# Performance work log

Measured on AMD Instinct MI355X. Metric: run time of the kernel, lower is better.

Reference implementation:

```python
import jax, jax.numpy as jnp
import numpy as np

N = 200000      # nodes (Elliptic-scale transaction graph)
E = 400000      # directed edges
F_IN = 165      # node features
HID = 128
OUT = 2


def setup_inputs() -> dict:
    key = jax.random.key(0)
    k = jax.random.split(key, 5)
    x = jax.random.normal(k[0], (N, F_IN), dtype=jnp.float32)
    edge_index = jax.random.randint(k[1], (2, E), 0, N, dtype=jnp.int32)
    # GCNConv params (PyG: Linear without bias semantics differ slightly by
    # version; here weight + bias, bias added after aggregation)
    W1 = jax.random.normal(k[2], (F_IN, HID), dtype=jnp.float32) * (1.0 / np.sqrt(F_IN))
    b1 = jnp.zeros((HID,), dtype=jnp.float32)
    W2 = jax.random.normal(k[3], (HID, OUT), dtype=jnp.float32) * (1.0 / np.sqrt(HID))
    b2 = jnp.zeros((OUT,), dtype=jnp.float32)
    return {"x": x, "edge_index": edge_index, "W1": W1, "b1": b1, "W2": W2, "b2": b2}


def _gcn_conv(h, edge_index, W, b):
    """PyG GCNConv: out = D^{-1/2} (A + I) D^{-1/2} (h @ W) + b."""
    h = h @ W                                    # [N, F_out]
    loop = jnp.arange(N, dtype=edge_index.dtype)
    src = jnp.concatenate([edge_index[0], loop])  # add self-loops
    dst = jnp.concatenate([edge_index[1], loop])
    # degree over destination nodes (self-loops guarantee deg >= 1)
    deg = jax.ops.segment_sum(jnp.ones_like(dst, dtype=h.dtype), dst, num_segments=N)
    dinv = jax.lax.rsqrt(deg)
    norm = dinv[src] * dinv[dst]                 # [E+N]
    msgs = h[src] * norm[:, None]                # gather + scale
    out = jax.ops.segment_sum(msgs, dst, num_segments=N)  # scatter-add
    return out + b


def reference(x, edge_index, W1, b1, W2, b2):
    h = _gcn_conv(x, edge_index, W1, b1)
    # torch.relu then F.dropout(training=False) (identity) then torch.relu:
    # in eval mode relu(relu(h)) == relu(h)
    h = jnp.maximum(h, 0.0)
    return _gcn_conv(h, edge_index, W2, b2)
```

## Files before the change

kernel.cpp:

```cpp
#include <hip/hip_runtime.h>
#include <hip/hip_bf16.h>

typedef __attribute__((ext_vector_type(8))) short bf16x8;
typedef __attribute__((ext_vector_type(4))) float f32x4;

#define N_NODES 200000
#define N_EDGES 400000
#define F_IN    165
#define HID     128
#define N_TILES 3125
#define KSTEPS  6
#define CAP     32

__device__ __forceinline__ uint bf16r(float f) {
  uint u = __float_as_uint(f);
  return (u + 0x7FFFu + ((u >> 16) & 1u)) >> 16;
}

__device__ __forceinline__ void gload16(const void* gp, void* lp) {
  __builtin_amdgcn_global_load_lds(
      (const __attribute__((address_space(1))) unsigned int*)gp,
      (__attribute__((address_space(3))) unsigned int*)lp, 16, 0, 0);
}


__global__ __launch_bounds__(256) void k_init(const float* __restrict__ W1,
                                              ushort* __restrict__ Wf,
                                              uint4* __restrict__ cursor) {
  int b = blockIdx.x;
  int tid = threadIdx.x;
  if (b < 96) {
    int id = b * 256 + tid;
    int j = id & 7;
    int lane = (id >> 3) & 63;
    int rem = id >> 9;
    int s = rem % 6;
    int ct = rem / 6;
    int k = s * 32 + (lane >> 4) * 8 + j;
    int col = ct * 16 + (lane & 15);
    float v = (k < F_IN) ? W1[k * HID + col] : 0.f;
    Wf[id] = (ushort)bf16r(v);
  } else {
    int i = (b - 96) * 256 + tid;
    if (i < 50000) cursor[i] = make_uint4(0, 0, 0, 0);
  }
}


__global__ __launch_bounds__(256) void k_gemm1p(const float* __restrict__ x,
                                                const ushort* __restrict__ Wf,
                                                const int* __restrict__ ei,
                                                int* __restrict__ cursor,
                                                int* __restrict__ slots,
                                                uint* __restrict__ g) {
  __shared__ float xs[64 * F_IN];
  const int tid  = threadIdx.x;
  const int wave = tid >> 6;
  const int lane = tid & 63;
  const int r15  = lane & 15;
  const int kg   = lane >> 4;

  if (tid < 128) {
    int e = blockIdx.x * 128 + tid;
    int d = ei[N_EDGES + e];
    int pos = atomicAdd(&cursor[d], 1);
    if (pos < CAP) slots[d * CAP + pos] = ei[e];
  }

  bf16x8 bfrag[2][KSTEPS];
  #pragma unroll
  for (int t = 0; t < 2; ++t) {
    int ct = wave * 2 + t;
    #pragma unroll
    for (int s = 0; s < KSTEPS; ++s)
      bfrag[t][s] = *(const bf16x8*)(Wf + (size_t)(((ct * KSTEPS + s) * 64 + lane) << 3));
  }

  const size_t tb = (size_t)blockIdx.x * (64 * F_IN);
  #pragma unroll
  for (int it = 0; it < 10; ++it) {
    gload16(x + tb + (size_t)(it * 256 + tid) * 4,
            (char*)xs + (size_t)(it * 256 + wave * 64) * 16);
  }
  if (tid < 80) {
    int c = 2560 + tid;
    *(float4*)((char*)xs + (size_t)c * 16) = *(const float4*)(x + tb + (size_t)c * 4);
  }
  __syncthreads();

  f32x4 acc[4][2];
  #pragma unroll
  for (int rg = 0; rg < 4; ++rg) {
    acc[rg][0] = (f32x4){0.f, 0.f, 0.f, 0.f};
    acc[rg][1] = (f32x4){0.f, 0.f, 0.f, 0.f};
  }

  #pragma unroll
  for (int rg = 0; rg < 4; ++rg) {
    const float* rp0 = xs + (rg * 16 + r15) * F_IN;
    #pragma unroll
    for (int s = 0; s < KSTEPS; ++s) {
      uint o0, o1, o2, o3;
      if (s < 5) {
        const float* rp = rp0 + s * 32 + kg * 8;
        o0 = bf16r(rp[0]) | (bf16r(rp[1]) << 16);
        o1 = bf16r(rp[2]) | (bf16r(rp[3]) << 16);
        o2 = bf16r(rp[4]) | (bf16r(rp[5]) << 16);
        o3 = bf16r(rp[6]) | (bf16r(rp[7]) << 16);
      } else {
        o0 = o1 = o2 = o3 = 0u;
        if (kg == 0) {
          const float* rp = rp0 + 160;
          o0 = bf16r(rp[0]) | (bf16r(rp[1]) << 16);
          o1 = bf16r(rp[2]) | (bf16r(rp[3]) << 16);
          o2 = bf16r(rp[4]);
        }
      }
      uint4 uu = make_uint4(o0, o1, o2, o3);
      bf16x8 a = *(bf16x8*)&uu;
      acc[rg][0] = __builtin_amdgcn_mfma_f32_16x16x32_bf16(a, bfrag[0][s], acc[rg][0], 0, 0, 0);
      acc[rg][1] = __builtin_amdgcn_mfma_f32_16x16x32_bf16(a, bfrag[1][s], acc[rg][1], 0, 0, 0);
    }
  }

  int base = blockIdx.x * 64;
  #pragma unroll
  for (int rg = 0; rg < 4; ++rg) {
    #pragma unroll
    for (int r = 0; r < 4; ++r) {
      int row = base + rg * 16 + kg * 4 + r;
      uint u = bf16r(acc[rg][0][r]) | (bf16r(acc[rg][1][r]) << 16);
      g[(size_t)row * 64 + wave * 16 + r15] = u;
    }
  }
}


__global__ __launch_bounds__(256) void k_agg1(const uint* __restrict__ g,
                                              const int* __restrict__ cursor,
                                              const int* __restrict__ slots,
                                              const float* __restrict__ b1,
                                              const float* __restrict__ W2,
                                              float* __restrict__ g2) {
  const int tid  = threadIdx.x;
  const int lane = tid & 63;
  const int wave = tid >> 6;
  const int sub  = lane >> 4;
  const int fl   = lane & 15;

  float  b1lo[4], b1hi[4];
  float2 w2lo[4], w2hi[4];
  #pragma unroll
  for (int k = 0; k < 4; ++k) {
    int dw = fl * 4 + k;
    int c0 = ((dw >> 4) << 5) + (dw & 15);
    b1lo[k] = b1[c0];
    b1hi[k] = b1[c0 + 16];
    w2lo[k] = *(const float2*)&W2[c0 * 2];
    w2hi[k] = *(const float2*)&W2[(c0 + 16) * 2];
  }

  int degs[8], slotv[8];
  #pragma unroll
  for (int it = 0; it < 8; ++it) {
    int node = blockIdx.x * 128 + it * 16 + wave * 4 + sub;
    int cn = min(node, N_NODES - 1);
    degs[it]  = cursor[cn];
    slotv[it] = slots[cn * CAP + fl];
  }

  #pragma unroll
  for (int it = 0; it < 8; ++it) {
    int node = blockIdx.x * 128 + it * 16 + wave * 4 + sub;
    if (node < N_NODES) {
      int deg = degs[it];
      float dv = rsqrtf(1.0f + (float)deg);
      int dcap = min(deg, 16);
      int srcl = (fl < dcap) ? slotv[it] : node;

      uint4 v = *(const uint4*)&g[(size_t)node * 64 + fl * 4];
      float sx0 = dv * __uint_as_float(v.x << 16), sy0 = dv * __uint_as_float(v.x & 0xFFFF0000u);
      float sx1 = dv * __uint_as_float(v.y << 16), sy1 = dv * __uint_as_float(v.y & 0xFFFF0000u);
      float sx2 = dv * __uint_as_float(v.z << 16), sy2 = dv * __uint_as_float(v.z & 0xFFFF0000u);
      float sx3 = dv * __uint_as_float(v.w << 16), sy3 = dv * __uint_as_float(v.w & 0xFFFF0000u);

      #pragma unroll
      for (int j = 0; j < 4; ++j) {
        int s = __shfl(srcl, sub * 16 + j);
        float wj = (j < dcap) ? rsqrtf(1.0f + (float)cursor[s]) : 0.f;
        uint4 w = *(const uint4*)&g[(size_t)s * 64 + fl * 4];
        sx0 = fmaf(__uint_as_float(w.x << 16), wj, sx0);
        sy0 = fmaf(__uint_as_float(w.x & 0xFFFF0000u), wj, sy0);
        sx1 = fmaf(__uint_as_float(w.y << 16), wj, sx1);
        sy1 = fmaf(__uint_as_float(w.y & 0xFFFF0000u), wj, sy1);
        sx2 = fmaf(__uint_as_float(w.z << 16), wj, sx2);
        sy2 = fmaf(__uint_as_float(w.z & 0xFFFF0000u), wj, sy2);
        sx3 = fmaf(__uint_as_float(w.w << 16), wj, sx3);
        sy3 = fmaf(__uint_as_float(w.w & 0xFFFF0000u), wj, sy3);
      }
      for (int j = 4; j < dcap; ++j) {
        int s = __shfl(srcl, sub * 16 + j);
        float wj = rsqrtf(1.0f + (float)cursor[s]);
        uint4 w = *(const uint4*)&g[(size_t)s * 64 + fl * 4];
        sx0 = fmaf(__uint_as_float(w.x << 16), wj, sx0);
        sy0 = fmaf(__uint_as_float(w.x & 0xFFFF0000u), wj, sy0);
        sx1 = fmaf(__uint_as_float(w.y << 16), wj, sx1);
        sy1 = fmaf(__uint_as_float(w.y & 0xFFFF0000u), wj, sy1);
        sx2 = fmaf(__uint_as_float(w.z << 16), wj, sx2);
        sy2 = fmaf(__uint_as_float(w.z & 0xFFFF0000u), wj, sy2);
        sx3 = fmaf(__uint_as_float(w.w << 16), wj, sx3);
        sy3 = fmaf(__uint_as_float(w.w & 0xFFFF0000u), wj, sy3);
      }
      for (int e = 16; e < min(deg, CAP); ++e) {
        int s = slots[node * CAP + e];
        float wj = rsqrtf(1.0f + (float)cursor[s]);
        uint4 w = *(const uint4*)&g[(size_t)s * 64 + fl * 4];
        sx0 = fmaf(__uint_as_float(w.x << 16), wj, sx0);
        sy0 = fmaf(__uint_as_float(w.x & 0xFFFF0000u), wj, sy0);
        sx1 = fmaf(__uint_as_float(w.y << 16), wj, sx1);
        sy1 = fmaf(__uint_as_float(w.y & 0xFFFF0000u), wj, sy1);
        sx2 = fmaf(__uint_as_float(w.z << 16), wj, sx2);
        sy2 = fmaf(__uint_as_float(w.z & 0xFFFF0000u), wj, sy2);
        sx3 = fmaf(__uint_as_float(w.w << 16), wj, sx3);
        sy3 = fmaf(__uint_as_float(w.w & 0xFFFF0000u), wj, sy3);
      }

      float h, p0 = 0.f, p1 = 0.f;
      h = fmaxf(fmaf(sx0, dv, b1lo[0]), 0.f); p0 = fmaf(h, w2lo[0].x, p0); p1 = fmaf(h, w2lo[0].y, p1);
      h = fmaxf(fmaf(sy0, dv, b1hi[0]), 0.f); p0 = fmaf(h, w2hi[0].x, p0); p1 = fmaf(h, w2hi[0].y, p1);
      h = fmaxf(fmaf(sx1, dv, b1lo[1]), 0.f); p0 = fmaf(h, w2lo[1].x, p0); p1 = fmaf(h, w2lo[1].y, p1);
      h = fmaxf(fmaf(sy1, dv, b1hi[1]), 0.f); p0 = fmaf(h, w2hi[1].x, p0); p1 = fmaf(h, w2hi[1].y, p1);
      h = fmaxf(fmaf(sx2, dv, b1lo[2]), 0.f); p0 = fmaf(h, w2lo[2].x, p0); p1 = fmaf(h, w2lo[2].y, p1);
      h = fmaxf(fmaf(sy2, dv, b1hi[2]), 0.f); p0 = fmaf(h, w2hi[2].x, p0); p1 = fmaf(h, w2hi[2].y, p1);
      h = fmaxf(fmaf(sx3, dv, b1lo[3]), 0.f); p0 = fmaf(h, w2lo[3].x, p0); p1 = fmaf(h, w2lo[3].y, p1);
      h = fmaxf(fmaf(sy3, dv, b1hi[3]), 0.f); p0 = fmaf(h, w2hi[3].x, p0); p1 = fmaf(h, w2hi[3].y, p1);

      #pragma unroll
      for (int off = 1; off < 16; off <<= 1) {
        p0 += __shfl_xor(p0, off);
        p1 += __shfl_xor(p1, off);
      }
      if (fl == 0) {
        *(float2*)&g2[(size_t)node * 2] = make_float2(p0 * dv, p1 * dv);
      }
    }
  }
}


__global__ __launch_bounds__(256) void k_agg2(const float2* __restrict__ g2,
                                              const int* __restrict__ cursor,
                                              const int* __restrict__ slots,
                                              const float* __restrict__ b2,
                                              float* __restrict__ out) {
  int i = blockIdx.x * 256 + threadIdx.x;
  if (i >= N_NODES) return;
  float2 s = g2[i];
  int deg = cursor[i];
  int dcap = min(deg, CAP);
  for (int e = 0; e < dcap; ++e) {
    float2 m = g2[slots[i * CAP + e]];
    s.x += m.x;
    s.y += m.y;
  }
  float dv = rsqrtf(1.0f + (float)deg);
  float2 o;
  o.x = fmaf(s.x, dv, b2[0]);
  o.y = fmaf(s.y, dv, b2[1]);
  *(float2*)&out[(size_t)i * 2] = o;
}


extern "C" void kernel_launch(void* const* d_in, const int* in_sizes, int n_in,
                              void* d_out, int out_size, void* d_ws, size_t ws_size,
                              hipStream_t stream) {
  const float* x  = (const float*)d_in[0];
  const int*   ei = (const int*)d_in[1];
  const float* W1 = (const float*)d_in[2];
  const float* b1 = (const float*)d_in[3];
  const float* W2 = (const float*)d_in[4];
  const float* b2 = (const float*)d_in[5];
  float* out = (float*)d_out;

  char* ws = (char*)d_ws;
  size_t off = 0;
  auto take = [&](size_t bytes) -> char* {
    char* p = ws + off;
    off = (off + bytes + 255) & ~(size_t)255;
    return p;
  };
  int*    cursor = (int*)   take((size_t)N_NODES * 4);
  int*    slots  = (int*)   take((size_t)N_NODES * CAP * 4);
  float*  g2     = (float*) take((size_t)N_NODES * 2 * 4);
  ushort* Wf     = (ushort*)take((size_t)8 * KSTEPS * 64 * 8 * 2);
  uint*   g      = (uint*)  take((size_t)N_NODES * 64 * 4);
  (void)ws_size; (void)in_sizes; (void)n_in; (void)out_size;

  k_init<<<292, 256, 0, stream>>>(W1, Wf, (uint4*)cursor);
  k_gemm1p<<<N_TILES, 256, 0, stream>>>(x, Wf, ei, cursor, slots, g);
  k_agg1<<<1563, 256, 0, stream>>>(g, cursor, slots, b1, W2, g2);
  k_agg2<<<(N_NODES + 255) / 256, 256, 0, stream>>>((const float2*)g2, cursor,
                                                    slots, b2, out);
}
```

Before: 102.8 us.

## Precast x to padded bf16 in a separate pass before the first GEMM

Measured after the change: 175.7 us. 70.9% more time.

```diff
diff --git a/kernel.cpp b/kernel.cpp
--- a/kernel.cpp
+++ b/kernel.cpp
@@ -8,8 +8,10 @@
 #define N_EDGES 400000
 #define F_IN    165
 #define HID     128
+#define BM      64
 #define N_TILES 3125
 #define KSTEPS  6
+#define PITCH   200
 #define CAP     32
 
 __device__ __forceinline__ uint bf16r(float f) {
@@ -24,36 +26,51 @@
 }
 
 
-__global__ __launch_bounds__(256) void k_init(const float* __restrict__ W1,
-                                              ushort* __restrict__ Wf,
-                                              uint4* __restrict__ cursor) {
-  int b = blockIdx.x;
-  int tid = threadIdx.x;
-  if (b < 96) {
-    int id = b * 256 + tid;
-    int j = id & 7;
-    int lane = (id >> 3) & 63;
-    int rem = id >> 9;
+__global__ __launch_bounds__(256) void k_xbf(const float* __restrict__ x,
+                                             ushort* __restrict__ xb,
+                                             const float* __restrict__ W1,
+                                             ushort* __restrict__ Wf,
+                                             uint4* __restrict__ cursor) {
+  int t = blockIdx.x * 256 + threadIdx.x;
+
+  if (t < 24576) {
+    int j = t & 7;
+    int lane = (t >> 3) & 63;
+    int rem = t >> 9;
     int s = rem % 6;
     int ct = rem / 6;
     int k = s * 32 + (lane >> 4) * 8 + j;
     int col = ct * 16 + (lane & 15);
     float v = (k < F_IN) ? W1[k * HID + col] : 0.f;
-    Wf[id] = (ushort)bf16r(v);
-  } else {
-    int i = (b - 96) * 256 + tid;
-    if (i < 50000) cursor[i] = make_uint4(0, 0, 0, 0);
-  }
-}
-
-
-__global__ __launch_bounds__(256) void k_gemm1p(const float* __restrict__ x,
+    Wf[t] = (ushort)bf16r(v);
+  }
+  if (t < 50000) cursor[t] = make_uint4(0, 0, 0, 0);
+
+  if (t < N_NODES * (PITCH / 8)) {
+    int row = t / (PITCH / 8);
+    int c8  = t - row * (PITCH / 8);
+    int kb  = c8 * 8;
+    const float* rp = x + (size_t)row * F_IN;
+    uint o[4];
+    #pragma unroll
+    for (int p = 0; p < 4; ++p) {
+      int k0 = kb + 2 * p;
+      uint lo = (k0     < F_IN) ? bf16r(rp[k0])     : 0u;
+      uint hi = (k0 + 1 < F_IN) ? bf16r(rp[k0 + 1]) : 0u;
+      o[p] = lo | (hi << 16);
+    }
+    *(uint4*)(xb + (size_t)row * PITCH + kb) = make_uint4(o[0], o[1], o[2], o[3]);
+  }
+}
+
+
+__global__ __launch_bounds__(256) void k_gemm1p(const ushort* __restrict__ xb,
                                                 const ushort* __restrict__ Wf,
                                                 const int* __restrict__ ei,
                                                 int* __restrict__ cursor,
                                                 int* __restrict__ slots,
                                                 uint* __restrict__ g) {
-  __shared__ float xs[64 * F_IN];
+  __shared__ ushort xs[BM * PITCH];
   const int tid  = threadIdx.x;
   const int wave = tid >> 6;
   const int lane = tid & 63;
@@ -76,15 +93,15 @@
       bfrag[t][s] = *(const bf16x8*)(Wf + (size_t)(((ct * KSTEPS + s) * 64 + lane) << 3));
   }
 
-  const size_t tb = (size_t)blockIdx.x * (64 * F_IN);
-  #pragma unroll
-  for (int it = 0; it < 10; ++it) {
-    gload16(x + tb + (size_t)(it * 256 + tid) * 4,
+  const size_t tb = (size_t)blockIdx.x * (BM * PITCH);
+  #pragma unroll
+  for (int it = 0; it < 6; ++it) {
+    gload16(xb + tb + (size_t)(it * 256 + tid) * 8,
             (char*)xs + (size_t)(it * 256 + wave * 64) * 16);
   }
-  if (tid < 80) {
-    int c = 2560 + tid;
-    *(float4*)((char*)xs + (size_t)c * 16) = *(const float4*)(x + tb + (size_t)c * 4);
+  if (tid < 64) {
+    int c = 1536 + tid;
+    *(uint4*)((char*)xs + (size_t)c * 16) = *(const uint4*)(xb + tb + (size_t)c * 8);
   }
   __syncthreads();
 
@@ -97,33 +114,16 @@
 
   #pragma unroll
   for (int rg = 0; rg < 4; ++rg) {
-    const float* rp0 = xs + (rg * 16 + r15) * F_IN;
+    const ushort* rp = xs + (rg * 16 + r15) * PITCH + kg * 8;
     #pragma unroll
     for (int s = 0; s < KSTEPS; ++s) {
-      uint o0, o1, o2, o3;
-      if (s < 5) {
-        const float* rp = rp0 + s * 32 + kg * 8;
-        o0 = bf16r(rp[0]) | (bf16r(rp[1]) << 16);
-        o1 = bf16r(rp[2]) | (bf16r(rp[3]) << 16);
-        o2 = bf16r(rp[4]) | (bf16r(rp[5]) << 16);
-        o3 = bf16r(rp[6]) | (bf16r(rp[7]) << 16);
-      } else {
-        o0 = o1 = o2 = o3 = 0u;
-        if (kg == 0) {
-          const float* rp = rp0 + 160;
-          o0 = bf16r(rp[0]) | (bf16r(rp[1]) << 16);
-          o1 = bf16r(rp[2]) | (bf16r(rp[3]) << 16);
-          o2 = bf16r(rp[4]);
-        }
-      }
-      uint4 uu = make_uint4(o0, o1, o2, o3);
-      bf16x8 a = *(bf16x8*)&uu;
+      bf16x8 a = *(const bf16x8*)(rp + s * 32);
       acc[rg][0] = __builtin_amdgcn_mfma_f32_16x16x32_bf16(a, bfrag[0][s], acc[rg][0], 0, 0, 0);
       acc[rg][1] = __builtin_amdgcn_mfma_f32_16x16x32_bf16(a, bfrag[1][s], acc[rg][1], 0, 0, 0);
     }
   }
 
-  int base = blockIdx.x * 64;
+  int base = blockIdx.x * BM;
   #pragma unroll
   for (int rg = 0; rg < 4; ++rg) {
     #pragma unroll
@@ -293,11 +293,13 @@
   int*    slots  = (int*)   take((size_t)N_NODES * CAP * 4);
   float*  g2     = (float*) take((size_t)N_NODES * 2 * 4);
   ushort* Wf     = (ushort*)take((size_t)8 * KSTEPS * 64 * 8 * 2);
+  ushort* xb     = (ushort*)take((size_t)N_NODES * PITCH * 2);
   uint*   g      = (uint*)  take((size_t)N_NODES * 64 * 4);
   (void)ws_size; (void)in_sizes; (void)n_in; (void)out_size;
 
-  k_init<<<292, 256, 0, stream>>>(W1, Wf, (uint4*)cursor);
-  k_gemm1p<<<N_TILES, 256, 0, stream>>>(x, Wf, ei, cursor, slots, g);
+  k_xbf<<<(N_NODES * (PITCH / 8) + 255) / 256, 256, 0, stream>>>(x, xb, W1, Wf,
+                                                                 (uint4*)cursor);
+  k_gemm1p<<<N_TILES, 256, 0, stream>>>(xb, Wf, ei, cursor, slots, g);
   k_agg1<<<1563, 256, 0, stream>>>(g, cursor, slots, b1, W2, g2);
   k_agg2<<<(N_NODES + 255) / 256, 256, 0, stream>>>((const float2*)g2, cursor,
                                                     slots, b2, out);
```
